# Kernel tuning notes

Hardware: AMD Instinct MI355X
Metric: run time of the kernel (lower is better)

## Reference

```python
import jax, jax.numpy as jnp
import numpy as np

N_NODES = 50000
N_EDGES = 25000
NNZ = 800000
IN_DIM = 256
OUT_DIM = 256


def setup_inputs() -> dict:
    key = jax.random.key(0)
    k1, k2, k3, k4, k5 = jax.random.split(key, 5)
    X = jax.random.normal(k1, (N_NODES, IN_DIM), dtype=jnp.float32)
    node_idx = jax.random.randint(k2, (NNZ,), 0, N_NODES, dtype=jnp.int64)
    edge_idx = jax.random.randint(k3, (NNZ,), 0, N_EDGES, dtype=jnp.int64)
    # Xavier-uniform-ish weight, zero bias (matches reset_parameters)
    limit = float(np.sqrt(6.0 / (IN_DIM + OUT_DIM)))
    W = jax.random.uniform(k4, (IN_DIM, OUT_DIM), dtype=jnp.float32, minval=-limit, maxval=limit)
    b = jnp.zeros((OUT_DIM,), dtype=jnp.float32)
    return {"X": X, "node_idx": node_idx, "edge_idx": edge_idx, "W": W, "b": b}


def reference(X, node_idx, edge_idx, W, b):
    # Y = X @ W + b  -- dense GEMM
    Y = X @ W + b  # [N, out_dim]

    ones = jnp.ones(node_idx.shape[0], dtype=Y.dtype)
    # D_v = rowsum(H)^-0.5 (inf -> 0); D_e = colsum(H)^-1 (inf -> 0)
    deg_v = jax.ops.segment_sum(ones, node_idx, num_segments=N_NODES)
    deg_e = jax.ops.segment_sum(ones, edge_idx, num_segments=N_EDGES)
    d_v = jnp.where(deg_v > 0, deg_v ** -0.5, 0.0)  # [N]
    d_e = jnp.where(deg_e > 0, 1.0 / deg_e, 0.0)    # [E]

    # step1 = H^T @ (D_v X): gather scaled node rows, scatter-add into edges
    Z = d_v[:, None] * Y                                   # [N, out_dim]
    step1 = jax.ops.segment_sum(Z[node_idx], edge_idx, num_segments=N_EDGES)  # [E, out_dim]
    # step2 = D_e @ step1
    step2 = d_e[:, None] * step1                           # [E, out_dim]
    # step3 = H @ step2: gather edge rows, scatter-add into nodes
    step3 = jax.ops.segment_sum(step2[edge_idx], node_idx, num_segments=N_NODES)  # [N, out_dim]
    # final = D_v @ step3
    return d_v[:, None] * step3
```

## Files before the change

### kernel.cpp

```cpp
#include <hip/hip_runtime.h>

#define N_NODES 50000
#define N_EDGES 25000
#define NNZ     800000
#define DIM     256

#define CAP_E 88
#define CAP_V 56

#define NBE 98
#define NBV 196
#define CE_COARSE 8800
#define CV_COARSE 4500
#define NNZ_PB 2048
#define P1_BLOCKS 391

#define B_A1   0
#define B_CE   0
#define B_CV   3449600
#define B_CSRE 12800000
#define B_CSRV 17200000
#define B_WT   22800000
#define B_CURV 22931072
#define B_CURE 23131072
#define B_S1B  23231072
#define B_CCUR 23331072
#define B_DV   23332248

typedef __attribute__((ext_vector_type(8))) short s8v;
typedef __attribute__((ext_vector_type(4))) float f4v;

__device__ __forceinline__ unsigned short f2bf(float f) {
    unsigned u = __float_as_uint(f);
    u = (u + 0x7FFFu + ((u >> 16) & 1u)) >> 16;
    return (unsigned short)u;
}
__device__ __forceinline__ float bf2f(unsigned short h) {
    return __uint_as_float(((unsigned)h) << 16);
}

__global__ __launch_bounds__(256) void k_prep(
        const float* __restrict__ X, const float* __restrict__ W,
        const int* __restrict__ node_idx, const int* __restrict__ edge_idx,
        unsigned short* __restrict__ Xb, unsigned short* __restrict__ WTb,
        unsigned* __restrict__ ccurE, unsigned* __restrict__ ccurV,
        unsigned* __restrict__ coarseE, unsigned* __restrict__ coarseV) {
    if (blockIdx.x < 6250) {
        size_t i = ((size_t)blockIdx.x * 256 + threadIdx.x) * 8;
        float4 p0 = *(const float4*)(X + i);
        float4 p1 = *(const float4*)(X + i + 4);
        unsigned short o[8] = {f2bf(p0.x), f2bf(p0.y), f2bf(p0.z), f2bf(p0.w),
                               f2bf(p1.x), f2bf(p1.y), f2bf(p1.z), f2bf(p1.w)};
        *(s8v*)(Xb + i) = *(const s8v*)o;
        return;
    }
    if (blockIdx.x < 6282) {
        int t = (blockIdx.x - 6250) * 256 + threadIdx.x;
        int n = t >> 5;
        int k0 = (t & 31) * 8;
        unsigned short o[8];
#pragma unroll
        for (int j = 0; j < 8; ++j) o[j] = f2bf(W[(size_t)(k0 + j) * DIM + n]);
        *(s8v*)(WTb + (size_t)n * DIM + k0) = *(const s8v*)o;
        return;
    }

    __shared__ unsigned histE[NBE], histV[NBV], baseE[NBE], baseV[NBV];
    const int tid = threadIdx.x;
    const int pb  = blockIdx.x - 6282;
    const int base = pb * NNZ_PB;

    if (tid < NBE) histE[tid] = 0;
    if (tid < NBV) histV[tid] = 0;
    __syncthreads();

    int idx0 = base + tid * 4;
    int idx1 = base + 1024 + tid * 4;
    bool ok0 = idx0 < NNZ, ok1 = idx1 < NNZ;
    int4 v0 = ok0 ? *(const int4*)(node_idx + idx0) : (int4){0,0,0,0};
    int4 e0 = ok0 ? *(const int4*)(edge_idx + idx0) : (int4){0,0,0,0};
    int4 v1 = ok1 ? *(const int4*)(node_idx + idx1) : (int4){0,0,0,0};
    int4 e1 = ok1 ? *(const int4*)(edge_idx + idx1) : (int4){0,0,0,0};
    int vv[8] = {v0.x, v0.y, v0.z, v0.w, v1.x, v1.y, v1.z, v1.w};
    int ee[8] = {e0.x, e0.y, e0.z, e0.w, e1.x, e1.y, e1.z, e1.w};

    unsigned short locE[8], locV[8];
#pragma unroll
    for (int j = 0; j < 8; ++j) {
        bool ok = (j < 4) ? ok0 : ok1;
        if (ok) {
            locE[j] = (unsigned short)atomicAdd(&histE[ee[j] >> 8], 1u);
            locV[j] = (unsigned short)atomicAdd(&histV[vv[j] >> 8], 1u);
        }
    }
    __syncthreads();
    if (tid < NBE) baseE[tid] = atomicAdd(&ccurE[tid], histE[tid]);
    if (tid < NBV) baseV[tid] = atomicAdd(&ccurV[tid], histV[tid]);
    __syncthreads();

#pragma unroll
    for (int j = 0; j < 8; ++j) {
        bool ok = (j < 4) ? ok0 : ok1;
        if (ok) {
            unsigned e = (unsigned)ee[j], v = (unsigned)vv[j];
            unsigned pe = baseE[e >> 8] + locE[j];
            if (pe < CE_COARSE)
                coarseE[(size_t)(e >> 8) * CE_COARSE + pe] = ((e & 255u) << 16) | v;
            unsigned pv = baseV[v >> 8] + locV[j];
            if (pv < CV_COARSE)
                coarseV[(size_t)(v >> 8) * CV_COARSE + pv] = ((v & 255u) << 16) | e;
        }
    }
}

__global__ __launch_bounds__(256) void k_fine(
        const unsigned* __restrict__ coarseE, const unsigned* __restrict__ coarseV,
        const unsigned* __restrict__ ccurE, const unsigned* __restrict__ ccurV,
        unsigned short* __restrict__ csrE, unsigned short* __restrict__ csrV,
        unsigned* __restrict__ cur_e, unsigned* __restrict__ cur_v,
        float* __restrict__ dv) {
    __shared__ unsigned cnt[256];
    __shared__ unsigned short slots[256 * CAP_E];
    const int tid = threadIdx.x;
    cnt[tid] = 0;
    __syncthreads();

    if (blockIdx.x < NBE) {
        int b = blockIdx.x;
        unsigned n = ccurE[b]; n = n < CE_COARSE ? n : CE_COARSE;
        const unsigned* src = coarseE + (size_t)b * CE_COARSE;
        for (unsigned i = tid; i < n; i += 256) {
            unsigned p = src[i];
            unsigned f = p >> 16, v = p & 0xFFFFu;
            unsigned pos = atomicAdd(&cnt[f], 1u);
            if (pos < CAP_E) slots[f * CAP_E + pos] = (unsigned short)v;
        }
        __syncthreads();
        int e = b * 256 + tid;
        if (e < N_EDGES) cur_e[e] = cnt[tid];
        int rows = N_EDGES - b * 256; rows = rows < 256 ? rows : 256;
        unsigned words = (unsigned)rows * (CAP_E / 2);
        unsigned* dst = (unsigned*)(csrE + (size_t)b * 256 * CAP_E);
        const unsigned* s = (const unsigned*)slots;
        for (unsigned i = tid; i < words; i += 256) dst[i] = s[i];
    } else {
        int b = blockIdx.x - NBE;
        unsigned n = ccurV[b]; n = n < CV_COARSE ? n : CV_COARSE;
        const unsigned* src = coarseV + (size_t)b * CV_COARSE;
        for (unsigned i = tid; i < n; i += 256) {
            unsigned p = src[i];
            unsigned f = p >> 16, e = p & 0xFFFFu;
            unsigned pos = atomicAdd(&cnt[f], 1u);
            if (pos < CAP_V) slots[f * CAP_V + pos] = (unsigned short)e;
        }
        __syncthreads();
        int v = b * 256 + tid;
        if (v < N_NODES) {
            unsigned c = cnt[tid];
            cur_v[v] = c;
            dv[v] = c ? __frsqrt_rn((float)c) : 0.0f;
        }
        int rows = N_NODES - b * 256; rows = rows < 256 ? rows : 256;
        unsigned words = (unsigned)rows * (CAP_V / 2);
        unsigned* dst = (unsigned*)(csrV + (size_t)b * 256 * CAP_V);
        const unsigned* s = (const unsigned*)slots;
        for (unsigned i = tid; i < words; i += 256) dst[i] = s[i];
    }
}

__global__ __launch_bounds__(256) void k_gather_edges(
        const unsigned short* __restrict__ Xb,
        const unsigned short* __restrict__ csrE,
        const unsigned* __restrict__ cur_e,
        const float* __restrict__ dv,
        unsigned short* __restrict__ A1, float* __restrict__ s1b) {
    int w = (blockIdx.x * 256 + threadIdx.x) >> 6;
    int lane = threadIdx.x & 63;
    if (w >= N_EDGES) return;
    unsigned cnt = cur_e[w]; cnt = cnt < CAP_E ? cnt : CAP_E;
    const unsigned short* lst = csrE + (size_t)w * CAP_E;
    float ax = 0.f, ay = 0.f, az = 0.f, aw = 0.f, ss = 0.f;
    unsigned j = 0;
    for (; j + 4 <= cnt; j += 4) {
        ushort4 ids = *(const ushort4*)(lst + j);
        int v0 = ids.x, v1 = ids.y, v2 = ids.z, v3 = ids.w;
        float s0 = dv[v0], s1 = dv[v1], s2 = dv[v2], s3 = dv[v3];
        ushort4 x0 = *(const ushort4*)(Xb + (size_t)v0 * DIM + lane * 4);
        ushort4 x1 = *(const ushort4*)(Xb + (size_t)v1 * DIM + lane * 4);
        ushort4 x2 = *(const ushort4*)(Xb + (size_t)v2 * DIM + lane * 4);
        ushort4 x3 = *(const ushort4*)(Xb + (size_t)v3 * DIM + lane * 4);
        ax = fmaf(s0, bf2f(x0.x), ax); ay = fmaf(s0, bf2f(x0.y), ay);
        az = fmaf(s0, bf2f(x0.z), az); aw = fmaf(s0, bf2f(x0.w), aw);
        ax = fmaf(s1, bf2f(x1.x), ax); ay = fmaf(s1, bf2f(x1.y), ay);
        az = fmaf(s1, bf2f(x1.z), az); aw = fmaf(s1, bf2f(x1.w), aw);
        ax = fmaf(s2, bf2f(x2.x), ax); ay = fmaf(s2, bf2f(x2.y), ay);
        az = fmaf(s2, bf2f(x2.z), az); aw = fmaf(s2, bf2f(x2.w), aw);
        ax = fmaf(s3, bf2f(x3.x), ax); ay = fmaf(s3, bf2f(x3.y), ay);
        az = fmaf(s3, bf2f(x3.z), az); aw = fmaf(s3, bf2f(x3.w), aw);
        ss += (s0 + s1) + (s2 + s3);
    }
    for (; j < cnt; ++j) {
        int v = lst[j];
        float s = dv[v];
        ushort4 x = *(const ushort4*)(Xb + (size_t)v * DIM + lane * 4);
        ax = fmaf(s, bf2f(x.x), ax); ay = fmaf(s, bf2f(x.y), ay);
        az = fmaf(s, bf2f(x.z), az); aw = fmaf(s, bf2f(x.w), aw);
        ss += s;
    }
    ushort4 o = {f2bf(ax), f2bf(ay), f2bf(az), f2bf(aw)};
    *(ushort4*)(A1 + (size_t)w * DIM + lane * 4) = o;
    if (lane == 0) s1b[w] = ss;
}

__global__ __launch_bounds__(256) void k_gemm_mfma(
        const unsigned short* __restrict__ A,
        const unsigned short* __restrict__ WT,
        const float* __restrict__ bias,
        const unsigned* __restrict__ cur_e,
        const float* __restrict__ s1b,
        unsigned short* __restrict__ S2) {
    const int tid  = threadIdx.x;
    const int wv   = tid >> 6;
    const int lane = tid & 63;
    const int quad = lane >> 4;
    const int l16  = lane & 15;
    const int r0   = blockIdx.x * 64;
    const int nb   = wv * 64;

    f4v acc[4][4];
#pragma unroll
    for (int mt = 0; mt < 4; ++mt)
#pragma unroll
        for (int nt = 0; nt < 4; ++nt) acc[mt][nt] = (f4v){0.f, 0.f, 0.f, 0.f};

    for (int k0 = 0; k0 < DIM; k0 += 32) {
        s8v a[4], b[4];
#pragma unroll
        for (int nt = 0; nt < 4; ++nt) {
            int n = nb + nt * 16 + l16;
            b[nt] = *(const s8v*)(WT + (size_t)n * DIM + k0 + quad * 8);
        }
#pragma unroll
        for (int mt = 0; mt < 4; ++mt) {
            int m = r0 + mt * 16 + l16;
            m = (m < N_EDGES) ? m : (N_EDGES - 1);
            a[mt] = *(const s8v*)(A + (size_t)m * DIM + k0 + quad * 8);
        }
#pragma unroll
        for (int mt = 0; mt < 4; ++mt)
#pragma unroll
            for (int nt = 0; nt < 4; ++nt)
                acc[mt][nt] = __builtin_amdgcn_mfma_f32_16x16x32_bf16(
                    a[mt], b[nt], acc[mt][nt], 0, 0, 0);
    }

    __syncthreads();

    float bv[4];
#pragma unroll
    for (int nt = 0; nt < 4; ++nt) bv[nt] = bias[nb + nt * 16 + l16];

#pragma unroll
    for (int mt = 0; mt < 4; ++mt) {
#pragma unroll
        for (int reg = 0; reg < 4; ++reg) {
            int row = r0 + mt * 16 + quad * 4 + reg;
            if (row < N_EDGES) {
                unsigned ce = cur_e[row];
                float sc = ce ? 1.0f / (float)ce : 0.0f;
                float sb = s1b[row];
#pragma unroll
                for (int nt = 0; nt < 4; ++nt) {
                    float v = sc * (acc[mt][nt][reg] + sb * bv[nt]);
                    S2[(size_t)row * DIM + nb + nt * 16 + l16] = f2bf(v);
                }
            }
        }
    }
}

__global__ __launch_bounds__(256) void k_gather_nodes(
        const unsigned short* __restrict__ S2,
        const unsigned short* __restrict__ csrV,
        const unsigned* __restrict__ cur_v,
        const float* __restrict__ dv,
        float* __restrict__ out) {
    int w = (blockIdx.x * 256 + threadIdx.x) >> 6;
    int lane = threadIdx.x & 63;
    if (w >= N_NODES) return;
    unsigned cnt = cur_v[w]; cnt = cnt < CAP_V ? cnt : CAP_V;
    const unsigned short* lst = csrV + (size_t)w * CAP_V;
    float ax = 0.f, ay = 0.f, az = 0.f, aw = 0.f;
    unsigned j = 0;
    for (; j + 4 <= cnt; j += 4) {
        ushort4 ids = *(const ushort4*)(lst + j);
        int e0 = ids.x, e1 = ids.y, e2 = ids.z, e3 = ids.w;
        ushort4 x0 = *(const ushort4*)(S2 + (size_t)e0 * DIM + lane * 4);
        ushort4 x1 = *(const ushort4*)(S2 + (size_t)e1 * DIM + lane * 4);
        ushort4 x2 = *(const ushort4*)(S2 + (size_t)e2 * DIM + lane * 4);
        ushort4 x3 = *(const ushort4*)(S2 + (size_t)e3 * DIM + lane * 4);
        ax += (bf2f(x0.x) + bf2f(x1.x)) + (bf2f(x2.x) + bf2f(x3.x));
        ay += (bf2f(x0.y) + bf2f(x1.y)) + (bf2f(x2.y) + bf2f(x3.y));
        az += (bf2f(x0.z) + bf2f(x1.z)) + (bf2f(x2.z) + bf2f(x3.z));
        aw += (bf2f(x0.w) + bf2f(x1.w)) + (bf2f(x2.w) + bf2f(x3.w));
    }
    for (; j < cnt; ++j) {
        int e = lst[j];
        ushort4 x = *(const ushort4*)(S2 + (size_t)e * DIM + lane * 4);
        ax += bf2f(x.x); ay += bf2f(x.y); az += bf2f(x.z); aw += bf2f(x.w);
    }
    float s = dv[w];
    float4 o = {s * ax, s * ay, s * az, s * aw};
    *(float4*)(out + (size_t)w * DIM + lane * 4) = o;
}

extern "C" void kernel_launch(void* const* d_in, const int* in_sizes, int n_in,
                              void* d_out, int out_size, void* d_ws, size_t ws_size,
                              hipStream_t stream) {
    (void)in_sizes; (void)n_in; (void)out_size; (void)ws_size;
    const float* X        = (const float*)d_in[0];
    const int*   node_idx = (const int*)d_in[1];
    const int*   edge_idx = (const int*)d_in[2];
    const float* W        = (const float*)d_in[3];
    const float* bias     = (const float*)d_in[4];
    float* out = (float*)d_out;
    char*  ws  = (char*)d_ws;

    unsigned short* A1      = (unsigned short*)(ws + B_A1);
    unsigned*       coarseE = (unsigned*)(ws + B_CE);
    unsigned*       coarseV = (unsigned*)(ws + B_CV);
    unsigned short* csrE    = (unsigned short*)(ws + B_CSRE);
    unsigned short* csrV    = (unsigned short*)(ws + B_CSRV);
    unsigned short* WTb     = (unsigned short*)(ws + B_WT);
    unsigned*       cur_v   = (unsigned*)(ws + B_CURV);
    unsigned*       cur_e   = (unsigned*)(ws + B_CURE);
    float*          s1b     = (float*)(ws + B_S1B);
    unsigned*       ccurE   = (unsigned*)(ws + B_CCUR);
    unsigned*       ccurV   = ccurE + NBE;
    float*          dv      = (float*)(ws + B_DV);

    unsigned short* Xb = (unsigned short*)d_out;

    hipMemsetAsync(ccurE, 0, (NBE + NBV) * sizeof(unsigned), stream);

    k_prep<<<6282 + P1_BLOCKS, 256, 0, stream>>>(X, W, node_idx, edge_idx,
                                                 Xb, WTb, ccurE, ccurV, coarseE, coarseV);
    k_fine<<<NBE + NBV, 256, 0, stream>>>(coarseE, coarseV, ccurE, ccurV,
                                          csrE, csrV, cur_e, cur_v, dv);
    k_gather_edges<<<(N_EDGES * 64 + 255) / 256, 256, 0, stream>>>(
        Xb, csrE, cur_e, dv, A1, s1b);
    k_gemm_mfma<<<(N_EDGES + 63) / 64, 256, 0, stream>>>(A1, WTb, bias, cur_e, s1b, A1);
    k_gather_nodes<<<(N_NODES * 64 + 255) / 256, 256, 0, stream>>>(
        A1, csrV, cur_v, dv, out);
}
```

Baseline: 272.1 us.

## Slice gather kernels by feature column and widen fine-bucketing blocks

Both gather kernels now split the 256-wide feature dimension into 8 column slices across blocks, with 16 lanes per row each loading 2 bf16 values. Consecutive blocks share a row tile, so each block's gathered working set is a narrow 64-byte column slice, which should improve cache locality. In exchange the index lists and dv values are reread 8 times, and each gathered access is a smaller 64-byte segment. The index lists now use nontemporal loads, the main loop unrolls 8 deep, and k_fine launches 1024 threads per block so its bucket scatter and copy-out run with more parallelism.

```diff
diff --git a/kernel.cpp b/kernel.cpp
--- a/kernel.cpp
+++ b/kernel.cpp
@@ -37,6 +37,15 @@
 }
 __device__ __forceinline__ float bf2f(unsigned short h) {
     return __uint_as_float(((unsigned)h) << 16);
+}
+__device__ __forceinline__ ushort4 nt_u4(const unsigned short* p) {
+    unsigned long long q = __builtin_nontemporal_load((const unsigned long long*)p);
+    ushort4 r;
+    r.x = (unsigned short)(q);
+    r.y = (unsigned short)(q >> 16);
+    r.z = (unsigned short)(q >> 32);
+    r.w = (unsigned short)(q >> 48);
+    return r;
 }
 
 __global__ __launch_bounds__(256) void k_prep(
@@ -113,7 +122,7 @@
     }
 }
 
-__global__ __launch_bounds__(256) void k_fine(
+__global__ __launch_bounds__(1024) void k_fine(
         const unsigned* __restrict__ coarseE, const unsigned* __restrict__ coarseV,
         const unsigned* __restrict__ ccurE, const unsigned* __restrict__ ccurV,
         unsigned short* __restrict__ csrE, unsigned short* __restrict__ csrV,
@@ -122,49 +131,53 @@
     __shared__ unsigned cnt[256];
     __shared__ unsigned short slots[256 * CAP_E];
     const int tid = threadIdx.x;
-    cnt[tid] = 0;
+    if (tid < 256) cnt[tid] = 0;
     __syncthreads();
 
     if (blockIdx.x < NBE) {
         int b = blockIdx.x;
         unsigned n = ccurE[b]; n = n < CE_COARSE ? n : CE_COARSE;
         const unsigned* src = coarseE + (size_t)b * CE_COARSE;
-        for (unsigned i = tid; i < n; i += 256) {
+        for (unsigned i = tid; i < n; i += 1024) {
             unsigned p = src[i];
             unsigned f = p >> 16, v = p & 0xFFFFu;
             unsigned pos = atomicAdd(&cnt[f], 1u);
             if (pos < CAP_E) slots[f * CAP_E + pos] = (unsigned short)v;
         }
         __syncthreads();
-        int e = b * 256 + tid;
-        if (e < N_EDGES) cur_e[e] = cnt[tid];
+        if (tid < 256) {
+            int e = b * 256 + tid;
+            if (e < N_EDGES) cur_e[e] = cnt[tid];
+        }
         int rows = N_EDGES - b * 256; rows = rows < 256 ? rows : 256;
         unsigned words = (unsigned)rows * (CAP_E / 2);
         unsigned* dst = (unsigned*)(csrE + (size_t)b * 256 * CAP_E);
         const unsigned* s = (const unsigned*)slots;
-        for (unsigned i = tid; i < words; i += 256) dst[i] = s[i];
+        for (unsigned i = tid; i < words; i += 1024) dst[i] = s[i];
     } else {
         int b = blockIdx.x - NBE;
         unsigned n = ccurV[b]; n = n < CV_COARSE ? n : CV_COARSE;
         const unsigned* src = coarseV + (size_t)b * CV_COARSE;
-        for (unsigned i = tid; i < n; i += 256) {
+        for (unsigned i = tid; i < n; i += 1024) {
             unsigned p = src[i];
             unsigned f = p >> 16, e = p & 0xFFFFu;
             unsigned pos = atomicAdd(&cnt[f], 1u);
             if (pos < CAP_V) slots[f * CAP_V + pos] = (unsigned short)e;
         }
         __syncthreads();
-        int v = b * 256 + tid;
-        if (v < N_NODES) {
-            unsigned c = cnt[tid];
-            cur_v[v] = c;
-            dv[v] = c ? __frsqrt_rn((float)c) : 0.0f;
+        if (tid < 256) {
+            int v = b * 256 + tid;
+            if (v < N_NODES) {
+                unsigned c = cnt[tid];
+                cur_v[v] = c;
+                dv[v] = c ? __frsqrt_rn((float)c) : 0.0f;
+            }
         }
         int rows = N_NODES - b * 256; rows = rows < 256 ? rows : 256;
         unsigned words = (unsigned)rows * (CAP_V / 2);
         unsigned* dst = (unsigned*)(csrV + (size_t)b * 256 * CAP_V);
         const unsigned* s = (const unsigned*)slots;
-        for (unsigned i = tid; i < words; i += 256) dst[i] = s[i];
+        for (unsigned i = tid; i < words; i += 1024) dst[i] = s[i];
     }
 }
 
@@ -174,42 +187,68 @@
         const unsigned* __restrict__ cur_e,
         const float* __restrict__ dv,
         unsigned short* __restrict__ A1, float* __restrict__ s1b) {
-    int w = (blockIdx.x * 256 + threadIdx.x) >> 6;
-    int lane = threadIdx.x & 63;
+    const int slice = blockIdx.x & 7;
+    const int tile  = blockIdx.x >> 3;
+    const int grp   = threadIdx.x >> 4;
+    const int l16   = threadIdx.x & 15;
+    int w = tile * 16 + grp;
     if (w >= N_EDGES) return;
     unsigned cnt = cur_e[w]; cnt = cnt < CAP_E ? cnt : CAP_E;
     const unsigned short* lst = csrE + (size_t)w * CAP_E;
-    float ax = 0.f, ay = 0.f, az = 0.f, aw = 0.f, ss = 0.f;
+    const unsigned short* xb  = Xb + slice * 32 + l16 * 2;
+
+    float a0 = 0.f, a1 = 0.f, ss = 0.f;
+
     unsigned j = 0;
-    for (; j + 4 <= cnt; j += 4) {
-        ushort4 ids = *(const ushort4*)(lst + j);
-        int v0 = ids.x, v1 = ids.y, v2 = ids.z, v3 = ids.w;
-        float s0 = dv[v0], s1 = dv[v1], s2 = dv[v2], s3 = dv[v3];
-        ushort4 x0 = *(const ushort4*)(Xb + (size_t)v0 * DIM + lane * 4);
-        ushort4 x1 = *(const ushort4*)(Xb + (size_t)v1 * DIM + lane * 4);
-        ushort4 x2 = *(const ushort4*)(Xb + (size_t)v2 * DIM + lane * 4);
-        ushort4 x3 = *(const ushort4*)(Xb + (size_t)v3 * DIM + lane * 4);
-        ax = fmaf(s0, bf2f(x0.x), ax); ay = fmaf(s0, bf2f(x0.y), ay);
-        az = fmaf(s0, bf2f(x0.z), az); aw = fmaf(s0, bf2f(x0.w), aw);
-        ax = fmaf(s1, bf2f(x1.x), ax); ay = fmaf(s1, bf2f(x1.y), ay);
-        az = fmaf(s1, bf2f(x1.z), az); aw = fmaf(s1, bf2f(x1.w), aw);
-        ax = fmaf(s2, bf2f(x2.x), ax); ay = fmaf(s2, bf2f(x2.y), ay);
-        az = fmaf(s2, bf2f(x2.z), az); aw = fmaf(s2, bf2f(x2.w), aw);
-        ax = fmaf(s3, bf2f(x3.x), ax); ay = fmaf(s3, bf2f(x3.y), ay);
-        az = fmaf(s3, bf2f(x3.z), az); aw = fmaf(s3, bf2f(x3.w), aw);
+    for (; j + 8 <= cnt; j += 8) {
+        ushort4 i0 = nt_u4(lst + j);
+        ushort4 i1 = nt_u4(lst + j + 4);
+        float s0 = dv[i0.x], s1 = dv[i0.y], s2 = dv[i0.z], s3 = dv[i0.w];
+        float t0 = dv[i1.x], t1 = dv[i1.y], t2 = dv[i1.z], t3 = dv[i1.w];
+        ushort2 x0 = *(const ushort2*)(xb + (size_t)i0.x * DIM);
+        ushort2 x1 = *(const ushort2*)(xb + (size_t)i0.y * DIM);
+        ushort2 x2 = *(const ushort2*)(xb + (size_t)i0.z * DIM);
+        ushort2 x3 = *(const ushort2*)(xb + (size_t)i0.w * DIM);
+        ushort2 x4 = *(const ushort2*)(xb + (size_t)i1.x * DIM);
+        ushort2 x5 = *(const ushort2*)(xb + (size_t)i1.y * DIM);
+        ushort2 x6 = *(const ushort2*)(xb + (size_t)i1.z * DIM);
+        ushort2 x7 = *(const ushort2*)(xb + (size_t)i1.w * DIM);
+        a0 = fmaf(s0, bf2f(x0.x), a0); a1 = fmaf(s0, bf2f(x0.y), a1);
+        a0 = fmaf(s1, bf2f(x1.x), a0); a1 = fmaf(s1, bf2f(x1.y), a1);
+        a0 = fmaf(s2, bf2f(x2.x), a0); a1 = fmaf(s2, bf2f(x2.y), a1);
+        a0 = fmaf(s3, bf2f(x3.x), a0); a1 = fmaf(s3, bf2f(x3.y), a1);
         ss += (s0 + s1) + (s2 + s3);
+        a0 = fmaf(t0, bf2f(x4.x), a0); a1 = fmaf(t0, bf2f(x4.y), a1);
+        a0 = fmaf(t1, bf2f(x5.x), a0); a1 = fmaf(t1, bf2f(x5.y), a1);
+        a0 = fmaf(t2, bf2f(x6.x), a0); a1 = fmaf(t2, bf2f(x6.y), a1);
+        a0 = fmaf(t3, bf2f(x7.x), a0); a1 = fmaf(t3, bf2f(x7.y), a1);
+        ss += (t0 + t1) + (t2 + t3);
+    }
+    if (j + 4 <= cnt) {
+        ushort4 i0 = nt_u4(lst + j);
+        float s0 = dv[i0.x], s1 = dv[i0.y], s2 = dv[i0.z], s3 = dv[i0.w];
+        ushort2 x0 = *(const ushort2*)(xb + (size_t)i0.x * DIM);
+        ushort2 x1 = *(const ushort2*)(xb + (size_t)i0.y * DIM);
+        ushort2 x2 = *(const ushort2*)(xb + (size_t)i0.z * DIM);
+        ushort2 x3 = *(const ushort2*)(xb + (size_t)i0.w * DIM);
+        a0 = fmaf(s0, bf2f(x0.x), a0); a1 = fmaf(s0, bf2f(x0.y), a1);
+        a0 = fmaf(s1, bf2f(x1.x), a0); a1 = fmaf(s1, bf2f(x1.y), a1);
+        a0 = fmaf(s2, bf2f(x2.x), a0); a1 = fmaf(s2, bf2f(x2.y), a1);
+        a0 = fmaf(s3, bf2f(x3.x), a0); a1 = fmaf(s3, bf2f(x3.y), a1);
+        ss += (s0 + s1) + (s2 + s3);
+        j += 4;
     }
     for (; j < cnt; ++j) {
-        int v = lst[j];
+        unsigned v = lst[j];
         float s = dv[v];
-        ushort4 x = *(const ushort4*)(Xb + (size_t)v * DIM + lane * 4);
-        ax = fmaf(s, bf2f(x.x), ax); ay = fmaf(s, bf2f(x.y), ay);
-        az = fmaf(s, bf2f(x.z), az); aw = fmaf(s, bf2f(x.w), aw);
+        ushort2 x = *(const ushort2*)(xb + (size_t)v * DIM);
+        a0 = fmaf(s, bf2f(x.x), a0); a1 = fmaf(s, bf2f(x.y), a1);
         ss += s;
     }
-    ushort4 o = {f2bf(ax), f2bf(ay), f2bf(az), f2bf(aw)};
-    *(ushort4*)(A1 + (size_t)w * DIM + lane * 4) = o;
-    if (lane == 0) s1b[w] = ss;
+
+    ushort2 o = {f2bf(a0), f2bf(a1)};
+    *(ushort2*)(A1 + (size_t)w * DIM + slice * 32 + l16 * 2) = o;
+    if (l16 == 0 && slice == 0) s1b[w] = ss;
 }
 
 __global__ __launch_bounds__(256) void k_gemm_mfma(
@@ -285,33 +324,54 @@
         const unsigned* __restrict__ cur_v,
         const float* __restrict__ dv,
         float* __restrict__ out) {
-    int w = (blockIdx.x * 256 + threadIdx.x) >> 6;
-    int lane = threadIdx.x & 63;
+    const int slice = blockIdx.x & 7;
+    const int tile  = blockIdx.x >> 3;
+    const int grp   = threadIdx.x >> 4;
+    const int l16   = threadIdx.x & 15;
+    int w = tile * 16 + grp;
     if (w >= N_NODES) return;
     unsigned cnt = cur_v[w]; cnt = cnt < CAP_V ? cnt : CAP_V;
     const unsigned short* lst = csrV + (size_t)w * CAP_V;
-    float ax = 0.f, ay = 0.f, az = 0.f, aw = 0.f;
+    const unsigned short* sb  = S2 + slice * 32 + l16 * 2;
+
+    float a0 = 0.f, a1 = 0.f;
+
     unsigned j = 0;
-    for (; j + 4 <= cnt; j += 4) {
-        ushort4 ids = *(const ushort4*)(lst + j);
-        int e0 = ids.x, e1 = ids.y, e2 = ids.z, e3 = ids.w;
-        ushort4 x0 = *(const ushort4*)(S2 + (size_t)e0 * DIM + lane * 4);
-        ushort4 x1 = *(const ushort4*)(S2 + (size_t)e1 * DIM + lane * 4);
-        ushort4 x2 = *(const ushort4*)(S2 + (size_t)e2 * DIM + lane * 4);
-        ushort4 x3 = *(const ushort4*)(S2 + (size_t)e3 * DIM + lane * 4);
-        ax += (bf2f(x0.x) + bf2f(x1.x)) + (bf2f(x2.x) + bf2f(x3.x));
-        ay += (bf2f(x0.y) + bf2f(x1.y)) + (bf2f(x2.y) + bf2f(x3.y));
-        az += (bf2f(x0.z) + bf2f(x1.z)) + (bf2f(x2.z) + bf2f(x3.z));
-        aw += (bf2f(x0.w) + bf2f(x1.w)) + (bf2f(x2.w) + bf2f(x3.w));
+    for (; j + 8 <= cnt; j += 8) {
+        ushort4 i0 = nt_u4(lst + j);
+        ushort4 i1 = nt_u4(lst + j + 4);
+        ushort2 x0 = *(const ushort2*)(sb + (size_t)i0.x * DIM);
+        ushort2 x1 = *(const ushort2*)(sb + (size_t)i0.y * DIM);
+        ushort2 x2 = *(const ushort2*)(sb + (size_t)i0.z * DIM);
+        ushort2 x3 = *(const ushort2*)(sb + (size_t)i0.w * DIM);
+        ushort2 x4 = *(const ushort2*)(sb + (size_t)i1.x * DIM);
+        ushort2 x5 = *(const ushort2*)(sb + (size_t)i1.y * DIM);
+        ushort2 x6 = *(const ushort2*)(sb + (size_t)i1.z * DIM);
+        ushort2 x7 = *(const ushort2*)(sb + (size_t)i1.w * DIM);
+        a0 += (bf2f(x0.x) + bf2f(x1.x)) + (bf2f(x2.x) + bf2f(x3.x));
+        a1 += (bf2f(x0.y) + bf2f(x1.y)) + (bf2f(x2.y) + bf2f(x3.y));
+        a0 += (bf2f(x4.x) + bf2f(x5.x)) + (bf2f(x6.x) + bf2f(x7.x));
+        a1 += (bf2f(x4.y) + bf2f(x5.y)) + (bf2f(x6.y) + bf2f(x7.y));
+    }
+    if (j + 4 <= cnt) {
+        ushort4 i0 = nt_u4(lst + j);
+        ushort2 x0 = *(const ushort2*)(sb + (size_t)i0.x * DIM);
+        ushort2 x1 = *(const ushort2*)(sb + (size_t)i0.y * DIM);
+        ushort2 x2 = *(const ushort2*)(sb + (size_t)i0.z * DIM);
+        ushort2 x3 = *(const ushort2*)(sb + (size_t)i0.w * DIM);
+        a0 += (bf2f(x0.x) + bf2f(x1.x)) + (bf2f(x2.x) + bf2f(x3.x));
+        a1 += (bf2f(x0.y) + bf2f(x1.y)) + (bf2f(x2.y) + bf2f(x3.y));
+        j += 4;
     }
     for (; j < cnt; ++j) {
-        int e = lst[j];
-        ushort4 x = *(const ushort4*)(S2 + (size_t)e * DIM + lane * 4);
-        ax += bf2f(x.x); ay += bf2f(x.y); az += bf2f(x.z); aw += bf2f(x.w);
-    }
+        unsigned e = lst[j];
+        ushort2 x = *(const ushort2*)(sb + (size_t)e * DIM);
+        a0 += bf2f(x.x); a1 += bf2f(x.y);
+    }
+
     float s = dv[w];
-    float4 o = {s * ax, s * ay, s * az, s * aw};
-    *(float4*)(out + (size_t)w * DIM + lane * 4) = o;
+    float2 o = {s * a0, s * a1};
+    *(float2*)(out + (size_t)w * DIM + slice * 32 + l16 * 2) = o;
 }
 
 extern "C" void kernel_launch(void* const* d_in, const int* in_sizes, int n_in,
@@ -341,15 +401,15 @@
 
     unsigned short* Xb = (unsigned short*)d_out;
 
-    hipMemsetAsync(ccurE, 0, (NBE + NBV) * sizeof(unsigned), stream);
+    (void)hipMemsetAsync(ccurE, 0, (NBE + NBV) * sizeof(unsigned), stream);
 
     k_prep<<<6282 + P1_BLOCKS, 256, 0, stream>>>(X, W, node_idx, edge_idx,
                                                  Xb, WTb, ccurE, ccurV, coarseE, coarseV);
-    k_fine<<<NBE + NBV, 256, 0, stream>>>(coarseE, coarseV, ccurE, ccurV,
-                                          csrE, csrV, cur_e, cur_v, dv);
-    k_gather_edges<<<(N_EDGES * 64 + 255) / 256, 256, 0, stream>>>(
+    k_fine<<<NBE + NBV, 1024, 0, stream>>>(coarseE, coarseV, ccurE, ccurV,
+                                           csrE, csrV, cur_e, cur_v, dv);
+    k_gather_edges<<<((N_EDGES + 15) / 16) * 8, 256, 0, stream>>>(
         Xb, csrE, cur_e, dv, A1, s1b);
     k_gemm_mfma<<<(N_EDGES + 63) / 64, 256, 0, stream>>>(A1, WTb, bias, cur_e, s1b, A1);
-    k_gather_nodes<<<(N_NODES * 64 + 255) / 256, 256, 0, stream>>>(
+    k_gather_nodes<<<((N_NODES + 15) / 16) * 8, 256, 0, stream>>>(
         A1, csrV, cur_v, dv, out);
 }
```

Measured after the change: 382.9 us. 1.41x slower.
